# Kernel tuning notes

Measured on AMD Instinct MI355X. Metric: run time of the kernel, lower is better.

Reference implementation:

```python
import jax, jax.numpy as jnp
import numpy as np

N = 100000      # nodes
E = 1600000     # edges (avg degree 16)
FEAT = 128
EMBED = 64
CLS = 40


def setup_inputs() -> dict:
    key = jax.random.key(0)
    k1, k2, k3, k4 = jax.random.split(key, 4)
    x = jax.random.normal(k1, (N, FEAT), dtype=jnp.float32)
    edge_index = jax.random.randint(k2, (2, E), 0, N, dtype=jnp.int32)
    W1 = jax.random.normal(k3, (FEAT, EMBED), dtype=jnp.float32) / np.sqrt(FEAT).astype(np.float32)
    b1 = jnp.zeros((EMBED,), dtype=jnp.float32)
    W2 = jax.random.normal(k4, (EMBED, CLS), dtype=jnp.float32) / np.sqrt(EMBED).astype(np.float32)
    b2 = jnp.zeros((CLS,), dtype=jnp.float32)
    return {"x": x, "edge_index": edge_index, "W1": W1, "b1": b1, "W2": W2, "b2": b2}


def gcn_conv(x, edge_index, W, b):
    """PyG GCNConv: linear -> add self loops -> symmetric-norm scatter-add -> bias."""
    n = x.shape[0]
    x = x @ W                                   # [n, out_dim]
    loops = jnp.arange(n, dtype=edge_index.dtype)
    row = jnp.concatenate([edge_index[0], loops])  # source nodes
    col = jnp.concatenate([edge_index[1], loops])  # destination nodes
    # degree after self-loops (in-degree over destination index)
    deg = jax.ops.segment_sum(jnp.ones_like(col, dtype=x.dtype), col, num_segments=n)
    dinv = jnp.where(deg > 0, jax.lax.rsqrt(deg), 0.0)
    norm = dinv[row] * dinv[col]                # [E+n]
    msg = x[row] * norm[:, None]                # gather + scale
    out = jax.ops.segment_sum(msg, col, num_segments=n)  # scatter-add
    return out + b


def reference(x, edge_index, W1, b1, W2, b2):
    h = jax.nn.relu(gcn_conv(x, edge_index, W1, b1))
    logits = gcn_conv(h, edge_index, W2, b2)
    return jax.nn.log_softmax(logits, axis=1)
```

## Files before the change

kernel.cpp:

```cpp
#include <hip/hip_runtime.h>
#include <math.h>

#define FEAT 128
#define EMBED 64
#define CLS 40

#define GRP 512
#define GSH 9
#define STRIDE 12288
#define T1 2048

typedef __attribute__((ext_vector_type(8))) short s8v;
typedef __attribute__((ext_vector_type(4))) float f32x4;

static __device__ __forceinline__ float bf2f(unsigned short u) {
    union { unsigned int i; float f; } c; c.i = ((unsigned int)u) << 16; return c.f;
}
static __device__ __forceinline__ unsigned short f2bf(float f) {
    union { float f; unsigned int i; } c; c.f = f;
    unsigned int x = c.i;
    x += 0x7fffu + ((x >> 16) & 1u);
    return (unsigned short)(x >> 16);
}


__global__ void k_initcur(int* __restrict__ cursor, int B) {
    int t = blockIdx.x * blockDim.x + threadIdx.x;
    if (t < B) cursor[t] = t * STRIDE;
}


__global__ __launch_bounds__(256) void k_p1(const int* __restrict__ ei,
                                            unsigned long long* __restrict__ pairs,
                                            int* __restrict__ cursor, int E, int B) {
    __shared__ unsigned long long pl[T1];
    __shared__ int hist[256], base[256], gbase[256], lcnt[256], scanbuf[256];
    int tid = threadIdx.x;
    int tile0 = blockIdx.x * T1;
    int cnt = min(T1, E - tile0);

    hist[tid] = 0; lcnt[tid] = 0;
    __syncthreads();

    int s[T1 / 256], d[T1 / 256];
#pragma unroll
    for (int i = 0; i < T1 / 256; ++i) {
        int k = i * 256 + tid;
        if (k < cnt) {
            s[i] = ei[tile0 + k];
            d[i] = ei[E + tile0 + k];
            atomicAdd(&hist[d[i] >> GSH], 1);
        }
    }
    __syncthreads();

    int h = hist[tid];
    scanbuf[tid] = h;
    __syncthreads();
    for (int off = 1; off < 256; off <<= 1) {
        int t = (tid >= (unsigned)off) ? scanbuf[tid - off] : 0;
        __syncthreads();
        scanbuf[tid] += t;
        __syncthreads();
    }
    base[tid] = scanbuf[tid] - h;
    gbase[tid] = (tid < B && h > 0) ? atomicAdd(&cursor[tid], h) : 0;
    __syncthreads();

#pragma unroll
    for (int i = 0; i < T1 / 256; ++i) {
        int k = i * 256 + tid;
        if (k < cnt) {
            int b = d[i] >> GSH;
            int pos = base[b] + atomicAdd(&lcnt[b], 1);
            pl[pos] = ((unsigned long long)(unsigned)d[i] << 32) | (unsigned)s[i];
        }
    }
    __syncthreads();

    for (int k = tid; k < cnt; k += 256) {
        unsigned long long p = pl[k];
        int b = (int)(p >> (32 + GSH));
        pairs[(size_t)gbase[b] + (k - base[b])] = p;
    }
}


__global__ void k_bscan(const int* __restrict__ cursor, int* __restrict__ csrBase,
                        int* __restrict__ rowptr, int B, int E, int N) {
    __shared__ int sh[256];
    int t = threadIdx.x;
    int c = (t < B) ? cursor[t] - t * STRIDE : 0;
    sh[t] = c;
    __syncthreads();
    for (int off = 1; off < 256; off <<= 1) {
        int u = (t >= off) ? sh[t - off] : 0;
        __syncthreads();
        sh[t] += u;
        __syncthreads();
    }
    if (t < B) csrBase[t] = sh[t] - c;
    if (t == 0) rowptr[N] = E;
}


__global__ __launch_bounds__(512) void k_p2(const unsigned long long* __restrict__ pairs,
                                            const int* __restrict__ cursor,
                                            const int* __restrict__ csrBase,
                                            int* __restrict__ csr, int* __restrict__ rowptr,
                                            float* __restrict__ dinv, int N) {
    __shared__ int hist[GRP], cur[GRP], scanbuf[GRP];
    int t = threadIdx.x;
    int b = blockIdx.x;
    int v0 = b << GSH;
    size_t reg0 = (size_t)b * STRIDE;
    int cnt = cursor[b] - b * STRIDE;

    hist[t] = 0;
    __syncthreads();
    for (int k = t; k < cnt; k += GRP)
        atomicAdd(&hist[(int)(pairs[reg0 + k] >> 32) - v0], 1);
    __syncthreads();

    int h = hist[t];
    scanbuf[t] = h;
    __syncthreads();
    for (int off = 1; off < GRP; off <<= 1) {
        int u = (t >= off) ? scanbuf[t - off] : 0;
        __syncthreads();
        scanbuf[t] += u;
        __syncthreads();
    }
    int excl = scanbuf[t] - h;
    int cB = csrBase[b];
    int v = v0 + t;
    if (v < N) {
        rowptr[v] = cB + excl;
        dinv[v] = rsqrtf((float)(h + 1));
    }
    cur[t] = excl;
    __syncthreads();

    for (int k = t; k < cnt; k += GRP) {
        unsigned long long p = pairs[reg0 + k];
        int l = (int)(p >> 32) - v0;
        int pos = atomicAdd(&cur[l], 1);
        csr[cB + pos] = (int)(p & 0xffffffffu);
    }
}


__global__ __launch_bounds__(256) void k_gemm1(const float* __restrict__ x,
                                               const float* __restrict__ W1,
                                               const float* __restrict__ dinv,
                                               unsigned short* __restrict__ A1, int N) {
    __shared__ unsigned short Wt[EMBED * 136];
    for (int i = threadIdx.x; i < FEAT * EMBED; i += 256) {
        int k = i >> 6, n = i & 63;
        Wt[n * 136 + k] = f2bf(W1[i]);
    }
    __syncthreads();

    int wv = threadIdx.x >> 6, lane = threadIdx.x & 63;
    int g = lane >> 4, r = lane & 15;
    int arow = blockIdx.x * 64 + wv * 16 + r;
    bool rowok = arow < N;
    float dv = rowok ? dinv[arow] : 0.f;

    s8v a[4];
#pragma unroll
    for (int ks = 0; ks < 4; ++ks) {
        if (rowok) {
            const float* p = x + (size_t)arow * FEAT + ks * 32 + g * 8;
            float4 p0 = *(const float4*)p;
            float4 p1 = *(const float4*)(p + 4);
            s8v t;
            t[0] = (short)f2bf(p0.x * dv); t[1] = (short)f2bf(p0.y * dv);
            t[2] = (short)f2bf(p0.z * dv); t[3] = (short)f2bf(p0.w * dv);
            t[4] = (short)f2bf(p1.x * dv); t[5] = (short)f2bf(p1.y * dv);
            t[6] = (short)f2bf(p1.z * dv); t[7] = (short)f2bf(p1.w * dv);
            a[ks] = t;
        } else {
            s8v z = {};
            a[ks] = z;
        }
    }

    f32x4 acc[4];
#pragma unroll
    for (int nt = 0; nt < 4; ++nt) acc[nt] = (f32x4){0.f, 0.f, 0.f, 0.f};

#pragma unroll
    for (int nt = 0; nt < 4; ++nt) {
        int n0 = nt * 16;
#pragma unroll
        for (int ks = 0; ks < 4; ++ks) {
            s8v bfr = *(const s8v*)&Wt[(n0 + r) * 136 + ks * 32 + g * 8];
            acc[nt] = __builtin_amdgcn_mfma_f32_16x16x32_bf16(a[ks], bfr, acc[nt], 0, 0, 0);
        }
    }

    int orow0 = blockIdx.x * 64 + wv * 16 + g * 4;
#pragma unroll
    for (int nt = 0; nt < 4; ++nt)
#pragma unroll
        for (int q = 0; q < 4; ++q) {
            int orow = orow0 + q;
            if (orow < N) A1[(size_t)orow * EMBED + nt * 16 + r] = f2bf(acc[nt][q]);
        }
}


struct I4 { int s0, s1, s2, s3; };
struct R4 { s8v u0, u1, u2, u3; };

static __device__ __forceinline__ I4 g_idx(const int* __restrict__ csr,
                                           int beg, int cnt, int v, int rs) {
    I4 r;
    r.s0 = (rs      < cnt - 1) ? csr[beg + rs]      : v;
    r.s1 = (rs + 8  < cnt - 1) ? csr[beg + rs + 8]  : v;
    r.s2 = (rs + 16 < cnt - 1) ? csr[beg + rs + 16] : v;
    r.s3 = (rs + 24 < cnt - 1) ? csr[beg + rs + 24] : v;
    return r;
}
static __device__ __forceinline__ R4 g_rows(const unsigned short* __restrict__ T,
                                            const I4& i, int dp) {
    R4 r;
    r.u0 = *(const s8v*)(T + (size_t)i.s0 * EMBED + dp);
    r.u1 = *(const s8v*)(T + (size_t)i.s1 * EMBED + dp);
    r.u2 = *(const s8v*)(T + (size_t)i.s2 * EMBED + dp);
    r.u3 = *(const s8v*)(T + (size_t)i.s3 * EMBED + dp);
    return r;
}
static __device__ __forceinline__ void accu(float* a, s8v u) {
#pragma unroll
    for (int i = 0; i < 8; ++i) a[i] += bf2f((unsigned short)u[i]);
}
static __device__ __forceinline__ void g_acc(const R4& r, int rs, int cnt, float* a) {
    if (rs < cnt)      accu(a, r.u0);
    if (rs + 8 < cnt)  accu(a, r.u1);
    if (rs + 16 < cnt) accu(a, r.u2);
    if (rs + 24 < cnt) accu(a, r.u3);
}
static __device__ __forceinline__ void g_tail(const unsigned short* __restrict__ T,
                                              const int* __restrict__ csr,
                                              int beg, int cnt, int v, int rs, int dp,
                                              float* a) {
    for (int p = 32 + rs; p < cnt; p += 8) {
        int s = (p < cnt - 1) ? csr[beg + p] : v;
        s8v u = *(const s8v*)(T + (size_t)s * EMBED + dp);
        accu(a, u);
    }
}
static __device__ __forceinline__ void fold8(float* a) {
#pragma unroll
    for (int o = 8; o < 64; o <<= 1) {
#pragma unroll
        for (int i = 0; i < 8; ++i) a[i] += __shfl_xor(a[i], o);
    }
}

__global__ __launch_bounds__(256) void k_gf1(const int* __restrict__ rowptr,
                                             const int* __restrict__ csr,
                                             const unsigned short* __restrict__ A1,
                                             const float* __restrict__ dinv,
                                             const float* __restrict__ b1,
                                             unsigned short* __restrict__ Hb, int N) {
    int wv = threadIdx.x >> 6, lane = threadIdx.x & 63;
    int va = (blockIdx.x * 4 + wv) * 2;
    if (va >= N) return;
    int vb = va + 1;
    bool okB = vb < N;
    int vB = okB ? vb : va;
    int rs = lane >> 3, dp = (lane & 7) * 8;

    int2 rp01 = *(const int2*)(rowptr + va);
    int rp2 = okB ? rowptr[vb + 1] : rp01.y;
    float dvA = dinv[va];
    float dvB = okB ? dinv[vb] : 0.f;
    float4 bL = *(const float4*)(b1 + dp);
    float4 bH = *(const float4*)(b1 + dp + 4);

    int begA = rp01.x, cntA = rp01.y - rp01.x + 1;
    int begB = rp01.y, cntB = okB ? (rp2 - rp01.y + 1) : 0;

    I4 iA = g_idx(csr, begA, cntA, va, rs);
    I4 iB = g_idx(csr, begB, cntB, vB, rs);
    R4 rA = g_rows(A1, iA, dp);
    R4 rB = g_rows(A1, iB, dp);

    float aA[8] = {0,0,0,0,0,0,0,0}, aB[8] = {0,0,0,0,0,0,0,0};
    g_acc(rA, rs, cntA, aA);
    g_acc(rB, rs, cntB, aB);
    if (cntA > 32) g_tail(A1, csr, begA, cntA, va, rs, dp, aA);
    if (cntB > 32) g_tail(A1, csr, begB, cntB, vB, rs, dp, aB);

    fold8(aA);
    fold8(aB);

    if (rs == 0) {
        s8v o;
        float h;
        h = fmaxf(dvA * aA[0] + bL.x, 0.f); o[0] = (short)f2bf(h * dvA);
        h = fmaxf(dvA * aA[1] + bL.y, 0.f); o[1] = (short)f2bf(h * dvA);
        h = fmaxf(dvA * aA[2] + bL.z, 0.f); o[2] = (short)f2bf(h * dvA);
        h = fmaxf(dvA * aA[3] + bL.w, 0.f); o[3] = (short)f2bf(h * dvA);
        h = fmaxf(dvA * aA[4] + bH.x, 0.f); o[4] = (short)f2bf(h * dvA);
        h = fmaxf(dvA * aA[5] + bH.y, 0.f); o[5] = (short)f2bf(h * dvA);
        h = fmaxf(dvA * aA[6] + bH.z, 0.f); o[6] = (short)f2bf(h * dvA);
        h = fmaxf(dvA * aA[7] + bH.w, 0.f); o[7] = (short)f2bf(h * dvA);
        *(s8v*)(Hb + (size_t)va * EMBED + dp) = o;
        if (okB) {
            s8v p;
            h = fmaxf(dvB * aB[0] + bL.x, 0.f); p[0] = (short)f2bf(h * dvB);
            h = fmaxf(dvB * aB[1] + bL.y, 0.f); p[1] = (short)f2bf(h * dvB);
            h = fmaxf(dvB * aB[2] + bL.z, 0.f); p[2] = (short)f2bf(h * dvB);
            h = fmaxf(dvB * aB[3] + bL.w, 0.f); p[3] = (short)f2bf(h * dvB);
            h = fmaxf(dvB * aB[4] + bH.x, 0.f); p[4] = (short)f2bf(h * dvB);
            h = fmaxf(dvB * aB[5] + bH.y, 0.f); p[5] = (short)f2bf(h * dvB);
            h = fmaxf(dvB * aB[6] + bH.z, 0.f); p[6] = (short)f2bf(h * dvB);
            h = fmaxf(dvB * aB[7] + bH.w, 0.f); p[7] = (short)f2bf(h * dvB);
            *(s8v*)(Hb + (size_t)vb * EMBED + dp) = p;
        }
    }
}

__global__ __launch_bounds__(256) void k_gf2h(const int* __restrict__ rowptr,
                                              const int* __restrict__ csr,
                                              const unsigned short* __restrict__ Hb,
                                              const float* __restrict__ dinv,
                                              unsigned short* __restrict__ Pb, int N) {
    int wv = threadIdx.x >> 6, lane = threadIdx.x & 63;
    int va = (blockIdx.x * 4 + wv) * 2;
    if (va >= N) return;
    int vb = va + 1;
    bool okB = vb < N;
    int vB = okB ? vb : va;
    int rs = lane >> 3, dp = (lane & 7) * 8;

    int2 rp01 = *(const int2*)(rowptr + va);
    int rp2 = okB ? rowptr[vb + 1] : rp01.y;
    float dvA = dinv[va];
    float dvB = okB ? dinv[vb] : 0.f;

    int begA = rp01.x, cntA = rp01.y - rp01.x + 1;
    int begB = rp01.y, cntB = okB ? (rp2 - rp01.y + 1) : 0;

    I4 iA = g_idx(csr, begA, cntA, va, rs);
    I4 iB = g_idx(csr, begB, cntB, vB, rs);
    R4 rA = g_rows(Hb, iA, dp);
    R4 rB = g_rows(Hb, iB, dp);

    float aA[8] = {0,0,0,0,0,0,0,0}, aB[8] = {0,0,0,0,0,0,0,0};
    g_acc(rA, rs, cntA, aA);
    g_acc(rB, rs, cntB, aB);
    if (cntA > 32) g_tail(Hb, csr, begA, cntA, va, rs, dp, aA);
    if (cntB > 32) g_tail(Hb, csr, begB, cntB, vB, rs, dp, aB);

    fold8(aA);
    fold8(aB);

    if (rs == 0) {
        s8v o;
#pragma unroll
        for (int i = 0; i < 8; ++i) o[i] = (short)f2bf(dvA * aA[i]);
        *(s8v*)(Pb + (size_t)va * EMBED + dp) = o;
        if (okB) {
            s8v p;
#pragma unroll
            for (int i = 0; i < 8; ++i) p[i] = (short)f2bf(dvB * aB[i]);
            *(s8v*)(Pb + (size_t)vb * EMBED + dp) = p;
        }
    }
}


__global__ __launch_bounds__(256) void k_fin(const unsigned short* __restrict__ Pb,
                                             const float* __restrict__ W2,
                                             const float* __restrict__ b2,
                                             float* __restrict__ out, int N) {
    __shared__ unsigned short Wt[48 * 72];
    for (int i = threadIdx.x; i < 48 * EMBED; i += 256) {
        int n = i >> 6, k = i & 63;
        Wt[n * 72 + k] = (n < CLS) ? f2bf(W2[k * CLS + n]) : 0;
    }
    __syncthreads();

    int wv = threadIdx.x >> 6, lane = threadIdx.x & 63;
    int g = lane >> 4, r = lane & 15;
    int arow = blockIdx.x * 64 + wv * 16 + r;

    s8v z = {};
    s8v a[2];
#pragma unroll
    for (int ks = 0; ks < 2; ++ks)
        a[ks] = (arow < N) ? *(const s8v*)(Pb + (size_t)arow * EMBED + ks * 32 + g * 8) : z;

    f32x4 acc[3];
#pragma unroll
    for (int nt = 0; nt < 3; ++nt) acc[nt] = (f32x4){0.f, 0.f, 0.f, 0.f};

#pragma unroll
    for (int nt = 0; nt < 3; ++nt)
#pragma unroll
        for (int ks = 0; ks < 2; ++ks) {
            s8v bfr = *(const s8v*)&Wt[(nt * 16 + r) * 72 + ks * 32 + g * 8];
            acc[nt] = __builtin_amdgcn_mfma_f32_16x16x32_bf16(a[ks], bfr, acc[nt], 0, 0, 0);
        }

    int orow0 = blockIdx.x * 64 + wv * 16 + g * 4;
    bool v2 = r < (CLS - 32);
#pragma unroll
    for (int q = 0; q < 4; ++q) {
        float l0 = acc[0][q] + b2[r];
        float l1 = acc[1][q] + b2[16 + r];
        float l2 = v2 ? acc[2][q] + b2[32 + r] : -INFINITY;
        float m = fmaxf(fmaxf(l0, l1), l2);
#pragma unroll
        for (int o = 1; o < 16; o <<= 1) m = fmaxf(m, __shfl_xor(m, o));
        float se = __expf(l0 - m) + __expf(l1 - m) + (v2 ? __expf(l2 - m) : 0.f);
#pragma unroll
        for (int o = 1; o < 16; o <<= 1) se += __shfl_xor(se, o);
        float lse = m + __logf(se);
        int orow = orow0 + q;
        if (orow < N) {
            float* op = out + (size_t)orow * CLS;
            op[r] = l0 - lse;
            op[16 + r] = l1 - lse;
            if (v2) op[32 + r] = l2 - lse;
        }
    }
}


extern "C" void kernel_launch(void* const* d_in, const int* in_sizes, int n_in,
                              void* d_out, int out_size, void* d_ws, size_t ws_size,
                              hipStream_t stream) {
    const float* x  = (const float*)d_in[0];
    const int*   ei = (const int*)d_in[1];
    const float* W1 = (const float*)d_in[2];
    const float* b1 = (const float*)d_in[3];
    const float* W2 = (const float*)d_in[4];
    const float* b2 = (const float*)d_in[5];
    float* out = (float*)d_out;

    const int N = in_sizes[0] / FEAT;
    const int E = in_sizes[1] / 2;
    const int B = (N + GRP - 1) >> GSH;

    char* ws = (char*)d_ws;
    size_t off = 0;
    auto alloc = [&](size_t bytes) { char* p = ws + off; off = (off + bytes + 255) & ~(size_t)255; return p; };
    int*   cursor  = (int*)alloc(256 * 4);
    int*   csrBase = (int*)alloc(256 * 4);
    float* dinv    = (float*)alloc((size_t)N * 4);
    int*   rowptr  = (int*)alloc((size_t)(N + 1) * 4);
    int*   csr     = (int*)alloc((size_t)E * 4);
    size_t regA = (size_t)B * STRIDE * 8;
    size_t regB = (size_t)N * EMBED * 4;
    char*  region = alloc(regA > regB ? regA : regB);
    unsigned long long* pairs = (unsigned long long*)region;
    unsigned short* A1 = (unsigned short*)region;
    unsigned short* Hb = (unsigned short*)(region + (size_t)N * EMBED * 2);
    unsigned short* Pb = A1;

    k_initcur<<<1, 256, 0, stream>>>(cursor, B);
    k_p1<<<(E + T1 - 1) / T1, 256, 0, stream>>>(ei, pairs, cursor, E, B);
    k_bscan<<<1, 256, 0, stream>>>(cursor, csrBase, rowptr, B, E, N);
    k_p2<<<B, GRP, 0, stream>>>(pairs, cursor, csrBase, csr, rowptr, dinv, N);

    k_gemm1<<<(N + 63) / 64, 256, 0, stream>>>(x, W1, dinv, A1, N);
    k_gf1<<<(N + 7) / 8, 256, 0, stream>>>(rowptr, csr, A1, dinv, b1, Hb, N);
    k_gf2h<<<(N + 7) / 8, 256, 0, stream>>>(rowptr, csr, Hb, dinv, Pb, N);
    k_fin<<<(N + 63) / 64, 256, 0, stream>>>(Pb, W2, b2, out, N);
}
```

Baseline: 142.3 us.

## Pack edge pairs into 32 bits and fuse second aggregation with W2 and log-softmax

Edge pairs in the binning pass are packed into one 32-bit word (9-bit local destination, 17-bit source) instead of 64 bits, which halves the pair scatter and read traffic. The second aggregation kernel now also does the W2 projection and log-softmax in fp32 from LDS, so the bf16 intermediate write/read and a kernel launch go away. The gathers now skip row loads for unused slots based on degree. The risks are a 17-bit source limit (N must stay at or below 131072), scalar LDS dot products in place of MFMA, an extra W2 load per block, and intra-wave LDS ordering that relies only on a waitcnt.

```diff
diff --git a/kernel.cpp b/kernel.cpp
--- a/kernel.cpp
+++ b/kernel.cpp
@@ -31,7 +31,7 @@
 
 
 __global__ __launch_bounds__(256) void k_p1(const int* __restrict__ ei,
-                                            unsigned long long* __restrict__ pairs,
+                                            unsigned int* __restrict__ pairs,
                                             int* __restrict__ cursor, int E, int B) {
     __shared__ unsigned long long pl[T1];
     __shared__ int hist[256], base[256], gbase[256], lcnt[256], scanbuf[256];
@@ -81,7 +81,9 @@
     for (int k = tid; k < cnt; k += 256) {
         unsigned long long p = pl[k];
         int b = (int)(p >> (32 + GSH));
-        pairs[(size_t)gbase[b] + (k - base[b])] = p;
+        unsigned int packed = (((unsigned int)(p >> 32) & (GRP - 1)) << 17)
+                            | ((unsigned int)p & 0x1FFFFu);
+        pairs[(size_t)gbase[b] + (k - base[b])] = packed;
     }
 }
 
@@ -104,7 +106,7 @@
 }
 
 
-__global__ __launch_bounds__(512) void k_p2(const unsigned long long* __restrict__ pairs,
+__global__ __launch_bounds__(512) void k_p2(const unsigned int* __restrict__ pairs,
                                             const int* __restrict__ cursor,
                                             const int* __restrict__ csrBase,
                                             int* __restrict__ csr, int* __restrict__ rowptr,
@@ -119,7 +121,7 @@
     hist[t] = 0;
     __syncthreads();
     for (int k = t; k < cnt; k += GRP)
-        atomicAdd(&hist[(int)(pairs[reg0 + k] >> 32) - v0], 1);
+        atomicAdd(&hist[pairs[reg0 + k] >> 17], 1);
     __syncthreads();
 
     int h = hist[t];
@@ -142,10 +144,10 @@
     __syncthreads();
 
     for (int k = t; k < cnt; k += GRP) {
-        unsigned long long p = pairs[reg0 + k];
-        int l = (int)(p >> 32) - v0;
+        unsigned int p = pairs[reg0 + k];
+        int l = p >> 17;
         int pos = atomicAdd(&cur[l], 1);
-        csr[cB + pos] = (int)(p & 0xffffffffu);
+        csr[cB + pos] = (int)(p & 0x1FFFFu);
     }
 }
 
@@ -212,7 +214,6 @@
 
 
 struct I4 { int s0, s1, s2, s3; };
-struct R4 { s8v u0, u1, u2, u3; };
 
 static __device__ __forceinline__ I4 g_idx(const int* __restrict__ csr,
                                            int beg, int cnt, int v, int rs) {
@@ -223,24 +224,9 @@
     r.s3 = (rs + 24 < cnt - 1) ? csr[beg + rs + 24] : v;
     return r;
 }
-static __device__ __forceinline__ R4 g_rows(const unsigned short* __restrict__ T,
-                                            const I4& i, int dp) {
-    R4 r;
-    r.u0 = *(const s8v*)(T + (size_t)i.s0 * EMBED + dp);
-    r.u1 = *(const s8v*)(T + (size_t)i.s1 * EMBED + dp);
-    r.u2 = *(const s8v*)(T + (size_t)i.s2 * EMBED + dp);
-    r.u3 = *(const s8v*)(T + (size_t)i.s3 * EMBED + dp);
-    return r;
-}
 static __device__ __forceinline__ void accu(float* a, s8v u) {
 #pragma unroll
     for (int i = 0; i < 8; ++i) a[i] += bf2f((unsigned short)u[i]);
-}
-static __device__ __forceinline__ void g_acc(const R4& r, int rs, int cnt, float* a) {
-    if (rs < cnt)      accu(a, r.u0);
-    if (rs + 8 < cnt)  accu(a, r.u1);
-    if (rs + 16 < cnt) accu(a, r.u2);
-    if (rs + 24 < cnt) accu(a, r.u3);
 }
 static __device__ __forceinline__ void g_tail(const unsigned short* __restrict__ T,
                                               const int* __restrict__ csr,
@@ -259,6 +245,32 @@
         for (int i = 0; i < 8; ++i) a[i] += __shfl_xor(a[i], o);
     }
 }
+
+#define GATHER2(TBL)                                                             \
+    I4 iA = g_idx(csr, begA, cntA, va, rs);                                      \
+    I4 iB = g_idx(csr, begB, cntB, vB, rs);                                      \
+    s8v uA0 = *(const s8v*)(TBL + (size_t)iA.s0 * EMBED + dp);                   \
+    s8v uB0 = *(const s8v*)(TBL + (size_t)iB.s0 * EMBED + dp);                   \
+    s8v uA1, uA2, uA3, uB1, uB2, uB3;                                            \
+    if (cntA > 8)  uA1 = *(const s8v*)(TBL + (size_t)iA.s1 * EMBED + dp);        \
+    if (cntB > 8)  uB1 = *(const s8v*)(TBL + (size_t)iB.s1 * EMBED + dp);        \
+    if (cntA > 16) uA2 = *(const s8v*)(TBL + (size_t)iA.s2 * EMBED + dp);        \
+    if (cntB > 16) uB2 = *(const s8v*)(TBL + (size_t)iB.s2 * EMBED + dp);        \
+    if (cntA > 24) uA3 = *(const s8v*)(TBL + (size_t)iA.s3 * EMBED + dp);        \
+    if (cntB > 24) uB3 = *(const s8v*)(TBL + (size_t)iB.s3 * EMBED + dp);        \
+    float aA[8] = {0,0,0,0,0,0,0,0}, aB[8] = {0,0,0,0,0,0,0,0};                  \
+    if (rs < cntA) accu(aA, uA0);                                                \
+    if (rs < cntB) accu(aB, uB0);                                                \
+    if (cntA > 8)  { if (rs + 8 < cntA)  accu(aA, uA1); }                        \
+    if (cntB > 8)  { if (rs + 8 < cntB)  accu(aB, uB1); }                        \
+    if (cntA > 16) { if (rs + 16 < cntA) accu(aA, uA2); }                        \
+    if (cntB > 16) { if (rs + 16 < cntB) accu(aB, uB2); }                        \
+    if (cntA > 24) { if (rs + 24 < cntA) accu(aA, uA3); }                        \
+    if (cntB > 24) { if (rs + 24 < cntB) accu(aB, uB3); }                        \
+    if (cntA > 32) g_tail(TBL, csr, begA, cntA, va, rs, dp, aA);                 \
+    if (cntB > 32) g_tail(TBL, csr, begB, cntB, vB, rs, dp, aB);                 \
+    fold8(aA);                                                                   \
+    fold8(aB);
 
 __global__ __launch_bounds__(256) void k_gf1(const int* __restrict__ rowptr,
                                              const int* __restrict__ csr,
@@ -284,19 +296,7 @@
     int begA = rp01.x, cntA = rp01.y - rp01.x + 1;
     int begB = rp01.y, cntB = okB ? (rp2 - rp01.y + 1) : 0;
 
-    I4 iA = g_idx(csr, begA, cntA, va, rs);
-    I4 iB = g_idx(csr, begB, cntB, vB, rs);
-    R4 rA = g_rows(A1, iA, dp);
-    R4 rB = g_rows(A1, iB, dp);
-
-    float aA[8] = {0,0,0,0,0,0,0,0}, aB[8] = {0,0,0,0,0,0,0,0};
-    g_acc(rA, rs, cntA, aA);
-    g_acc(rB, rs, cntB, aB);
-    if (cntA > 32) g_tail(A1, csr, begA, cntA, va, rs, dp, aA);
-    if (cntB > 32) g_tail(A1, csr, begB, cntB, vB, rs, dp, aB);
-
-    fold8(aA);
-    fold8(aB);
+    GATHER2(A1)
 
     if (rs == 0) {
         s8v o;
@@ -325,11 +325,18 @@
     }
 }
 
-__global__ __launch_bounds__(256) void k_gf2h(const int* __restrict__ rowptr,
-                                              const int* __restrict__ csr,
-                                              const unsigned short* __restrict__ Hb,
-                                              const float* __restrict__ dinv,
-                                              unsigned short* __restrict__ Pb, int N) {
+__global__ __launch_bounds__(256) void k_gf2(const int* __restrict__ rowptr,
+                                             const int* __restrict__ csr,
+                                             const unsigned short* __restrict__ Hb,
+                                             const float* __restrict__ dinv,
+                                             const float* __restrict__ W2,
+                                             const float* __restrict__ b2,
+                                             float* __restrict__ out, int N) {
+    __shared__ float W2l[EMBED * CLS];
+    __shared__ float Plds[4][2][EMBED];
+    for (int i = threadIdx.x; i < EMBED * CLS; i += 256) W2l[i] = W2[i];
+    __syncthreads();
+
     int wv = threadIdx.x >> 6, lane = threadIdx.x & 63;
     int va = (blockIdx.x * 4 + wv) * 2;
     if (va >= N) return;
@@ -346,89 +353,40 @@
     int begA = rp01.x, cntA = rp01.y - rp01.x + 1;
     int begB = rp01.y, cntB = okB ? (rp2 - rp01.y + 1) : 0;
 
-    I4 iA = g_idx(csr, begA, cntA, va, rs);
-    I4 iB = g_idx(csr, begB, cntB, vB, rs);
-    R4 rA = g_rows(Hb, iA, dp);
-    R4 rB = g_rows(Hb, iB, dp);
-
-    float aA[8] = {0,0,0,0,0,0,0,0}, aB[8] = {0,0,0,0,0,0,0,0};
-    g_acc(rA, rs, cntA, aA);
-    g_acc(rB, rs, cntB, aB);
-    if (cntA > 32) g_tail(Hb, csr, begA, cntA, va, rs, dp, aA);
-    if (cntB > 32) g_tail(Hb, csr, begB, cntB, vB, rs, dp, aB);
-
-    fold8(aA);
-    fold8(aB);
+    GATHER2(Hb)
 
     if (rs == 0) {
-        s8v o;
-#pragma unroll
-        for (int i = 0; i < 8; ++i) o[i] = (short)f2bf(dvA * aA[i]);
-        *(s8v*)(Pb + (size_t)va * EMBED + dp) = o;
-        if (okB) {
-            s8v p;
-#pragma unroll
-            for (int i = 0; i < 8; ++i) p[i] = (short)f2bf(dvB * aB[i]);
-            *(s8v*)(Pb + (size_t)vb * EMBED + dp) = p;
-        }
-    }
-}
-
-
-__global__ __launch_bounds__(256) void k_fin(const unsigned short* __restrict__ Pb,
-                                             const float* __restrict__ W2,
-                                             const float* __restrict__ b2,
-                                             float* __restrict__ out, int N) {
-    __shared__ unsigned short Wt[48 * 72];
-    for (int i = threadIdx.x; i < 48 * EMBED; i += 256) {
-        int n = i >> 6, k = i & 63;
-        Wt[n * 72 + k] = (n < CLS) ? f2bf(W2[k * CLS + n]) : 0;
-    }
-    __syncthreads();
-
-    int wv = threadIdx.x >> 6, lane = threadIdx.x & 63;
-    int g = lane >> 4, r = lane & 15;
-    int arow = blockIdx.x * 64 + wv * 16 + r;
-
-    s8v z = {};
-    s8v a[2];
-#pragma unroll
-    for (int ks = 0; ks < 2; ++ks)
-        a[ks] = (arow < N) ? *(const s8v*)(Pb + (size_t)arow * EMBED + ks * 32 + g * 8) : z;
-
-    f32x4 acc[3];
-#pragma unroll
-    for (int nt = 0; nt < 3; ++nt) acc[nt] = (f32x4){0.f, 0.f, 0.f, 0.f};
-
-#pragma unroll
-    for (int nt = 0; nt < 3; ++nt)
-#pragma unroll
-        for (int ks = 0; ks < 2; ++ks) {
-            s8v bfr = *(const s8v*)&Wt[(nt * 16 + r) * 72 + ks * 32 + g * 8];
-            acc[nt] = __builtin_amdgcn_mfma_f32_16x16x32_bf16(a[ks], bfr, acc[nt], 0, 0, 0);
-        }
-
-    int orow0 = blockIdx.x * 64 + wv * 16 + g * 4;
-    bool v2 = r < (CLS - 32);
-#pragma unroll
-    for (int q = 0; q < 4; ++q) {
-        float l0 = acc[0][q] + b2[r];
-        float l1 = acc[1][q] + b2[16 + r];
-        float l2 = v2 ? acc[2][q] + b2[32 + r] : -INFINITY;
-        float m = fmaxf(fmaxf(l0, l1), l2);
-#pragma unroll
-        for (int o = 1; o < 16; o <<= 1) m = fmaxf(m, __shfl_xor(m, o));
-        float se = __expf(l0 - m) + __expf(l1 - m) + (v2 ? __expf(l2 - m) : 0.f);
-#pragma unroll
-        for (int o = 1; o < 16; o <<= 1) se += __shfl_xor(se, o);
-        float lse = m + __logf(se);
-        int orow = orow0 + q;
-        if (orow < N) {
-            float* op = out + (size_t)orow * CLS;
-            op[r] = l0 - lse;
-            op[16 + r] = l1 - lse;
-            if (v2) op[32 + r] = l2 - lse;
-        }
+        int q = lane & 7;
+#pragma unroll
+        for (int i = 0; i < 8; ++i) {
+            Plds[wv][0][q * 8 + i] = dvA * aA[i];
+            Plds[wv][1][q * 8 + i] = dvB * aB[i];
+        }
+    }
+    __asm__ volatile("s_waitcnt lgkmcnt(0)" ::: "memory");
+    __builtin_amdgcn_sched_barrier(0);
+
+    float bias = (lane < CLS) ? b2[lane] : 0.f;
+#pragma unroll
+    for (int n = 0; n < 2; ++n) {
+        if (n == 1 && !okB) break;
+        int v = (n == 0) ? va : vb;
+        float logit = -INFINITY;
+        if (lane < CLS) {
+            float acc = bias;
+#pragma unroll 8
+            for (int k = 0; k < EMBED; ++k)
+                acc += Plds[wv][n][k] * W2l[k * CLS + lane];
+            logit = acc;
+        }
+        float m = logit;
+#pragma unroll
+        for (int o = 32; o > 0; o >>= 1) m = fmaxf(m, __shfl_xor(m, o));
+        float ex = (lane < CLS) ? __expf(logit - m) : 0.f;
+        float se = ex;
+#pragma unroll
+        for (int o = 32; o > 0; o >>= 1) se += __shfl_xor(se, o);
+        if (lane < CLS) out[(size_t)v * CLS + lane] = logit - m - __logf(se);
     }
 }
 
@@ -456,13 +414,12 @@
     float* dinv    = (float*)alloc((size_t)N * 4);
     int*   rowptr  = (int*)alloc((size_t)(N + 1) * 4);
     int*   csr     = (int*)alloc((size_t)E * 4);
-    size_t regA = (size_t)B * STRIDE * 8;
+    size_t regA = (size_t)B * STRIDE * 4;
     size_t regB = (size_t)N * EMBED * 4;
     char*  region = alloc(regA > regB ? regA : regB);
-    unsigned long long* pairs = (unsigned long long*)region;
+    unsigned int*   pairs = (unsigned int*)region;
     unsigned short* A1 = (unsigned short*)region;
     unsigned short* Hb = (unsigned short*)(region + (size_t)N * EMBED * 2);
-    unsigned short* Pb = A1;
 
     k_initcur<<<1, 256, 0, stream>>>(cursor, B);
     k_p1<<<(E + T1 - 1) / T1, 256, 0, stream>>>(ei, pairs, cursor, E, B);
@@ -471,6 +428,5 @@
 
     k_gemm1<<<(N + 63) / 64, 256, 0, stream>>>(x, W1, dinv, A1, N);
     k_gf1<<<(N + 7) / 8, 256, 0, stream>>>(rowptr, csr, A1, dinv, b1, Hb, N);
-    k_gf2h<<<(N + 7) / 8, 256, 0, stream>>>(rowptr, csr, Hb, dinv, Pb, N);
-    k_fin<<<(N + 63) / 64, 256, 0, stream>>>(Pb, W2, b2, out, N);
-}
+    k_gf2<<<(N + 7) / 8, 256, 0, stream>>>(rowptr, csr, Hb, dinv, W2, b2, out, N);
+}
```

Result: slower. 214.9 us (+51.0%).
